# Kernel optimization log

Measured on AMD Instinct MI355X. Metric: run time of the kernel, lower is better.

## Reference

```python
import jax, jax.numpy as jnp
import numpy as np

EPSILON = 1e-6
SEARCH_RADIUS = 11 // 2  # search_window_size=11 -> 121 shifts
PATCH_RADIUS = 5 // 2    # patch_size=5 box sum


def shift_stack(t, r):
    # Matches ShiftStack: outer loop x_shift, inner loop y_shift, roll dims (H,W)=(2,3).
    # t: [B,C,H,W] -> [B,C,H,W,(2r+1)^2]
    return jnp.stack(
        [jnp.roll(t, (dy, dx), axis=(2, 3))
         for dx in range(-r, r + 1) for dy in range(-r, r + 1)],
        axis=-1,
    )


def box_sum(t, r):
    # Circular box-filter sum over a (2r+1)x(2r+1) window; separable form is
    # mathematically identical to the original 25 rolls (rolls commute/add).
    s = sum(jnp.roll(t, d, axis=2) for d in range(-r, r + 1))
    return sum(jnp.roll(s, d, axis=3) for d in range(-r, r + 1))


def setup_inputs() -> dict:
    key = jax.random.key(0)
    k1, k2 = jax.random.split(key)
    rgb = jax.random.uniform(k1, (1, 3, 512, 512), dtype=jnp.float32)
    # realistic noise std in [0.02, 0.12]
    sigma = jax.random.uniform(k2, (1, 1, 1, 1), dtype=jnp.float32) * 0.1 + 0.02
    return {"rgb": rgb, "sigma": sigma}


def reference(rgb, sigma):
    h = sigma * 2.0                                     # [B,1,1,1]
    y = 0.299 * rgb[:, :1] + 0.587 * rgb[:, 1:2] + 0.114 * rgb[:, 2:]  # [B,1,H,W]
    rgb_stack = shift_stack(rgb, SEARCH_RADIUS)         # [B,3,H,W,K]
    y_stack = shift_stack(y, SEARCH_RADIUS)             # [B,1,H,W,K]
    sq_diff = (y[..., None] - y_stack) ** 2             # [B,1,H,W,K]
    distances = jnp.sqrt(box_sum(sq_diff, PATCH_RADIUS))
    weights = jnp.exp(-distances / (jax.nn.relu(h)[..., None] + EPSILON))  # [B,1,H,W,K]
    denoised = (weights * rgb_stack).sum(axis=-1) / weights.sum(axis=-1)   # [B,3,H,W]
    return jnp.clip(denoised, 0.0, 1.0)
```

## Files before the change

### kernel.cpp

```cpp
#include <hip/hip_runtime.h>
#include <math.h>

#define IH 512
#define IW 512
#define NPX (IH*IW)
#define TS 32
#define YHALO 7
#define RHALO 5
#define YD (TS + 2*YHALO)
#define RD (TS + 2*RHALO)
#define RSZ (RD*RD)
#define NSLICE 4

#define FSQRT(x) __builtin_amdgcn_sqrtf(x)

__global__ __launch_bounds__(256)
void nlm_part(const float* __restrict__ rgb,
              const float* __restrict__ sigma,
              float4* __restrict__ ws) {
    __shared__ float Y[YD * YD];
    __shared__ float RGBL[3 * RSZ];

    const int tid = threadIdx.x;
    const int tx0 = blockIdx.x * TS;
    const int ty0 = blockIdx.y * TS;
    const int slice = blockIdx.z;

    const float* Rp = rgb;
    const float* Gp = rgb + NPX;
    const float* Bp = rgb + 2 * NPX;

    for (int idx = tid; idx < YD * YD; idx += 256) {
        int a = idx / YD, b = idx - a * YD;
        int gy = (ty0 + a - YHALO) & (IH - 1);
        int gx = (tx0 + b - YHALO) & (IW - 1);
        int g = gy * IW + gx;
        Y[idx] = 0.299f * Rp[g] + 0.587f * Gp[g] + 0.114f * Bp[g];
    }
    for (int idx = tid; idx < RSZ; idx += 256) {
        int a = idx / RD, b = idx - a * RD;
        int gy = (ty0 + a - RHALO) & (IH - 1);
        int gx = (tx0 + b - RHALO) & (IW - 1);
        int g = gy * IW + gx;
        RGBL[idx]           = Rp[g];
        RGBL[RSZ + idx]     = Gp[g];
        RGBL[2 * RSZ + idx] = Bp[g];
    }
    __syncthreads();

    const float minv_h = -1.0f / (fmaxf(sigma[0] * 2.0f, 0.0f) + 1e-6f);

    const int tx = tid & 31;
    const int tz = tid >> 5;
    const int r0 = tz * 4;

    const int ybase = (YHALO + r0 - 2) * YD + (YHALO + tx - 2);
    float yb[8][5];
    #pragma unroll
    for (int i = 0; i < 8; ++i)
        #pragma unroll
        for (int b = 0; b < 5; ++b)
            yb[i][b] = Y[ybase + i * YD + b];

    float accR[4] = {0.f, 0.f, 0.f, 0.f};
    float accG[4] = {0.f, 0.f, 0.f, 0.f};
    float accB[4] = {0.f, 0.f, 0.f, 0.f};
    float den[4]  = {0.f, 0.f, 0.f, 0.f};

    const int dxlo  = (slice < 3) ? (-5 + 3 * slice) : 4;
    const int dxcnt = (slice < 3) ? 3 : 2;

    for (int u = 0; u < dxcnt; ++u) {
        const int dx = dxlo + u;
        const int ybd = (YHALO + r0 - 7) * YD + (YHALO + tx - 2 - dx);
        const int rbd = (RHALO + r0 - 5) * RD + (RHALO + tx - dx);

        float win[8][5];
        #pragma unroll
        for (int j = 0; j < 8; ++j)
            #pragma unroll
            for (int b = 0; b < 5; ++b)
                win[j][b] = Y[ybd + j * YD + b];

        #pragma unroll
        for (int k = 0; k <= 10; ++k) {
            if (k > 0) {
                #pragma unroll
                for (int b = 0; b < 5; ++b)
                    win[(k + 7) & 7][b] = Y[ybd + (7 + k) * YD + b];
            }
            float hs[8];
            #pragma unroll
            for (int i = 0; i < 8; ++i) {
                float s = 0.f;
                #pragma unroll
                for (int b = 0; b < 5; ++b) {
                    float d = yb[i][b] - win[(i + k) & 7][b];
                    s = fmaf(d, d, s);
                }
                hs[i] = s;
            }
            float pre[9];
            pre[0] = 0.f;
            #pragma unroll
            for (int i = 0; i < 8; ++i) pre[i + 1] = pre[i] + hs[i];
            #pragma unroll
            for (int rr = 0; rr < 4; ++rr) {
                float box = pre[rr + 5] - pre[rr];
                float w = __expf(FSQRT(box) * minv_h);
                const int s2 = rbd + (rr + k) * RD;
                accR[rr] = fmaf(w, RGBL[s2], accR[rr]);
                accG[rr] = fmaf(w, RGBL[RSZ + s2], accG[rr]);
                accB[rr] = fmaf(w, RGBL[2 * RSZ + s2], accB[rr]);
                den[rr] += w;
            }
        }
    }

    #pragma unroll
    for (int rr = 0; rr < 4; ++rr) {
        int px = (ty0 + r0 + rr) * IW + tx0 + tx;
        ws[(size_t)slice * NPX + px] =
            make_float4(accR[rr], accG[rr], accB[rr], den[rr]);
    }
}

__global__ __launch_bounds__(256)
void nlm_combine(const float4* __restrict__ ws, float* __restrict__ out) {
    int px = blockIdx.x * 256 + threadIdx.x;
    float4 a = ws[px];
    float4 b = ws[NPX + px];
    float4 c = ws[2 * (size_t)NPX + px];
    float4 d = ws[3 * (size_t)NPX + px];
    float r  = a.x + b.x + c.x + d.x;
    float g  = a.y + b.y + c.y + d.y;
    float bl = a.z + b.z + c.z + d.z;
    float w  = a.w + b.w + c.w + d.w;
    float iw = 1.0f / w;
    out[px]               = fminf(fmaxf(r  * iw, 0.f), 1.f);
    out[NPX + px]         = fminf(fmaxf(g  * iw, 0.f), 1.f);
    out[2 * NPX + px]     = fminf(fmaxf(bl * iw, 0.f), 1.f);
}

__global__ __launch_bounds__(256)
void nlm_mono(const float* __restrict__ rgb,
              const float* __restrict__ sigma,
              float* __restrict__ out) {
    __shared__ float Y[YD * YD];
    __shared__ float RGBL[3 * RSZ];

    const int tid = threadIdx.x;
    const int tx0 = blockIdx.x * TS;
    const int ty0 = blockIdx.y * TS;

    const float* Rp = rgb;
    const float* Gp = rgb + NPX;
    const float* Bp = rgb + 2 * NPX;

    for (int idx = tid; idx < YD * YD; idx += 256) {
        int a = idx / YD, b = idx - a * YD;
        int gy = (ty0 + a - YHALO) & (IH - 1);
        int gx = (tx0 + b - YHALO) & (IW - 1);
        int g = gy * IW + gx;
        Y[idx] = 0.299f * Rp[g] + 0.587f * Gp[g] + 0.114f * Bp[g];
    }
    for (int idx = tid; idx < RSZ; idx += 256) {
        int a = idx / RD, b = idx - a * RD;
        int gy = (ty0 + a - RHALO) & (IH - 1);
        int gx = (tx0 + b - RHALO) & (IW - 1);
        int g = gy * IW + gx;
        RGBL[idx]           = Rp[g];
        RGBL[RSZ + idx]     = Gp[g];
        RGBL[2 * RSZ + idx] = Bp[g];
    }
    __syncthreads();

    const float minv_h = -1.0f / (fmaxf(sigma[0] * 2.0f, 0.0f) + 1e-6f);
    const int tx = tid & 31;
    const int tz = tid >> 5;
    const int r0 = tz * 4;

    const int ybase = (YHALO + r0 - 2) * YD + (YHALO + tx - 2);
    float yb[8][5];
    #pragma unroll
    for (int i = 0; i < 8; ++i)
        #pragma unroll
        for (int b = 0; b < 5; ++b)
            yb[i][b] = Y[ybase + i * YD + b];

    float accR[4] = {0.f,0.f,0.f,0.f}, accG[4] = {0.f,0.f,0.f,0.f};
    float accB[4] = {0.f,0.f,0.f,0.f}, den[4] = {0.f,0.f,0.f,0.f};

    for (int dx = -5; dx <= 5; ++dx) {
        const int ybd = (YHALO + r0 - 7) * YD + (YHALO + tx - 2 - dx);
        const int rbd = (RHALO + r0 - 5) * RD + (RHALO + tx - dx);

        float win[8][5];
        #pragma unroll
        for (int j = 0; j < 8; ++j)
            #pragma unroll
            for (int b = 0; b < 5; ++b)
                win[j][b] = Y[ybd + j * YD + b];

        #pragma unroll
        for (int k = 0; k <= 10; ++k) {
            if (k > 0) {
                #pragma unroll
                for (int b = 0; b < 5; ++b)
                    win[(k + 7) & 7][b] = Y[ybd + (7 + k) * YD + b];
            }
            float hs[8];
            #pragma unroll
            for (int i = 0; i < 8; ++i) {
                float s = 0.f;
                #pragma unroll
                for (int b = 0; b < 5; ++b) {
                    float d = yb[i][b] - win[(i + k) & 7][b];
                    s = fmaf(d, d, s);
                }
                hs[i] = s;
            }
            float pre[9];
            pre[0] = 0.f;
            #pragma unroll
            for (int i = 0; i < 8; ++i) pre[i + 1] = pre[i] + hs[i];
            #pragma unroll
            for (int rr = 0; rr < 4; ++rr) {
                float box = pre[rr + 5] - pre[rr];
                float w = __expf(FSQRT(box) * minv_h);
                const int s2 = rbd + (rr + k) * RD;
                accR[rr] = fmaf(w, RGBL[s2], accR[rr]);
                accG[rr] = fmaf(w, RGBL[RSZ + s2], accG[rr]);
                accB[rr] = fmaf(w, RGBL[2 * RSZ + s2], accB[rr]);
                den[rr] += w;
            }
        }
    }

    #pragma unroll
    for (int rr = 0; rr < 4; ++rr) {
        int px = (ty0 + r0 + rr) * IW + tx0 + tx;
        float iw = 1.0f / den[rr];
        out[px]           = fminf(fmaxf(accR[rr] * iw, 0.f), 1.f);
        out[NPX + px]     = fminf(fmaxf(accG[rr] * iw, 0.f), 1.f);
        out[2 * NPX + px] = fminf(fmaxf(accB[rr] * iw, 0.f), 1.f);
    }
}

extern "C" void kernel_launch(void* const* d_in, const int* in_sizes, int n_in,
                              void* d_out, int out_size, void* d_ws, size_t ws_size,
                              hipStream_t stream) {
    const float* rgb   = (const float*)d_in[0];
    const float* sigma = (const float*)d_in[1];
    float* out = (float*)d_out;

    const size_t need = (size_t)NSLICE * NPX * sizeof(float4);
    if (ws_size >= need) {
        float4* ws = (float4*)d_ws;
        dim3 grid(IW / TS, IH / TS, NSLICE);
        nlm_part<<<grid, dim3(256), 0, stream>>>(rgb, sigma, ws);
        nlm_combine<<<dim3(NPX / 256), dim3(256), 0, stream>>>(ws, out);
    } else {
        dim3 grid(IW / TS, IH / TS);
        nlm_mono<<<grid, dim3(256), 0, stream>>>(rgb, sigma, out);
    }
}
```

Baseline: 42.52 us.

## Expand squared difference into correlation, use float2 LDS reads and more slices

The patch SSD is rewritten as |a|^2+|b|^2-2ab, with the query norms precomputed and the window norms computed incrementally. Window values are read from shared memory as float2 using even and odd shifted copies of the luma tile. RGB values now come straight from global memory (cached) instead of an LDS tile. The dx split grows to 6 slices when workspace allows, exp is replaced by exp2 with a prescaled constant, and the combine kernel takes a variable slice count. The expansion can lose precision through cancellation, so the box sum is clamped at zero, and the extra slices add partial-sum traffic.

After: 62.08 us. +46.0%, slower.

```diff
diff --git a/kernel.cpp b/kernel.cpp
--- a/kernel.cpp
+++ b/kernel.cpp
@@ -10,27 +10,171 @@
 #define YD (TS + 2*YHALO)
 #define RD (TS + 2*RHALO)
 #define RSZ (RD*RD)
-#define NSLICE 4
+#define YSZ (YD*YD)
 
 #define FSQRT(x) __builtin_amdgcn_sqrtf(x)
+#if __has_builtin(__builtin_amdgcn_exp2f)
+#define FEXP2(x) __builtin_amdgcn_exp2f(x)
+#else
+#define FEXP2(x) exp2f(x)
+#endif
 
 __global__ __launch_bounds__(256)
 void nlm_part(const float* __restrict__ rgb,
               const float* __restrict__ sigma,
               float4* __restrict__ ws) {
-    __shared__ float Y[YD * YD];
-    __shared__ float RGBL[3 * RSZ];
+    __shared__ float Ye[YSZ];
+    __shared__ float Yo[YSZ];
 
     const int tid = threadIdx.x;
     const int tx0 = blockIdx.x * TS;
     const int ty0 = blockIdx.y * TS;
     const int slice = blockIdx.z;
+    const int nz = gridDim.z;
 
     const float* Rp = rgb;
     const float* Gp = rgb + NPX;
     const float* Bp = rgb + 2 * NPX;
 
-    for (int idx = tid; idx < YD * YD; idx += 256) {
+    for (int idx = tid; idx < YSZ; idx += 256) {
+        int a = idx / YD, b = idx - a * YD;
+        int gy = (ty0 + a - YHALO) & (IH - 1);
+        int gx = (tx0 + b - YHALO) & (IW - 1);
+        int g = gy * IW + gx;
+        float y = 0.299f * Rp[g] + 0.587f * Gp[g] + 0.114f * Bp[g];
+        Ye[idx] = y;
+        if (b > 0) Yo[idx - 1] = y;
+    }
+    __syncthreads();
+
+    const float m2 = -1.4426950408889634f /
+                     (fmaxf(sigma[0] * 2.0f, 0.0f) + 1e-6f);
+
+    const int tx = tid & 31;
+    const int tz = tid >> 5;
+    const int r0 = tz * 4;
+
+    const int ybase = (YHALO + r0 - 2) * YD + (YHALO + tx - 2);
+    float yb[8][5];
+    float ybsq[8];
+    #pragma unroll
+    for (int i = 0; i < 8; ++i) {
+        float s = 0.f;
+        #pragma unroll
+        for (int b = 0; b < 5; ++b) {
+            float v = Ye[ybase + i * YD + b];
+            yb[i][b] = v;
+            s = fmaf(v, v, s);
+        }
+        ybsq[i] = s;
+    }
+
+    int rb[14];
+    #pragma unroll
+    for (int q = 0; q < 14; ++q)
+        rb[q] = ((ty0 + r0 - 5 + q) & (IH - 1)) << 9;
+
+    float accR[4] = {0.f, 0.f, 0.f, 0.f};
+    float accG[4] = {0.f, 0.f, 0.f, 0.f};
+    float accB[4] = {0.f, 0.f, 0.f, 0.f};
+    float den[4]  = {0.f, 0.f, 0.f, 0.f};
+
+    int dxlo, dxcnt;
+    if (nz == 6) { if (slice < 5) { dxlo = -5 + 2 * slice; dxcnt = 2; }
+                   else           { dxlo = 5;              dxcnt = 1; } }
+    else         { if (slice < 3) { dxlo = -5 + 3 * slice; dxcnt = 3; }
+                   else           { dxlo = 4;              dxcnt = 2; } }
+
+    for (int u = 0; u < dxcnt; ++u) {
+        const int dx  = dxlo + u;
+        const int col = (tx0 + tx - dx) & (IW - 1);
+        const int c   = YHALO + tx - 2 - dx;
+        const float* Yb_ = (c & 1) ? Yo : Ye;
+        const int ci  = (c & 1) ? (c - 1) : c;
+        const float2* wbase =
+            reinterpret_cast<const float2*>(Yb_ + r0 * YD + ci);
+
+        float winsq[8];
+        #pragma unroll
+        for (int k = 0; k <= 10; ++k) {
+            float hs[8];
+            #pragma unroll
+            for (int i = 0; i < 8; ++i) {
+                const int j = i + k;
+                float2 w0 = wbase[j * (YD / 2) + 0];
+                float2 w1 = wbase[j * (YD / 2) + 1];
+                float2 w2 = wbase[j * (YD / 2) + 2];
+                float cr = yb[i][0] * w0.x;
+                cr = fmaf(yb[i][1], w0.y, cr);
+                cr = fmaf(yb[i][2], w1.x, cr);
+                cr = fmaf(yb[i][3], w1.y, cr);
+                cr = fmaf(yb[i][4], w2.x, cr);
+                if (k == 0 || i == 7) {
+                    float s = w0.x * w0.x;
+                    s = fmaf(w0.y, w0.y, s);
+                    s = fmaf(w1.x, w1.x, s);
+                    s = fmaf(w1.y, w1.y, s);
+                    s = fmaf(w2.x, w2.x, s);
+                    winsq[j & 7] = s;
+                }
+                hs[i] = fmaf(-2.f, cr, ybsq[i] + winsq[j & 7]);
+            }
+            float pre[9];
+            pre[0] = 0.f;
+            #pragma unroll
+            for (int i = 0; i < 8; ++i) pre[i + 1] = pre[i] + hs[i];
+            #pragma unroll
+            for (int rr = 0; rr < 4; ++rr) {
+                float box = fmaxf(pre[rr + 5] - pre[rr], 0.f);
+                float w = FEXP2(FSQRT(box) * m2);
+                const int off = rb[rr + k] + col;
+                accR[rr] = fmaf(w, Rp[off], accR[rr]);
+                accG[rr] = fmaf(w, Gp[off], accG[rr]);
+                accB[rr] = fmaf(w, Bp[off], accB[rr]);
+                den[rr] += w;
+            }
+        }
+    }
+
+    #pragma unroll
+    for (int rr = 0; rr < 4; ++rr) {
+        int px = (ty0 + r0 + rr) * IW + tx0 + tx;
+        ws[(size_t)slice * NPX + px] =
+            make_float4(accR[rr], accG[rr], accB[rr], den[rr]);
+    }
+}
+
+__global__ __launch_bounds__(256)
+void nlm_combine(const float4* __restrict__ ws, float* __restrict__ out,
+                 int nslice) {
+    int px = blockIdx.x * 256 + threadIdx.x;
+    float r = 0.f, g = 0.f, b = 0.f, w = 0.f;
+    for (int s = 0; s < nslice; ++s) {
+        float4 v = ws[(size_t)s * NPX + px];
+        r += v.x; g += v.y; b += v.z; w += v.w;
+    }
+    float iw = 1.0f / w;
+    out[px]           = fminf(fmaxf(r * iw, 0.f), 1.f);
+    out[NPX + px]     = fminf(fmaxf(g * iw, 0.f), 1.f);
+    out[2 * NPX + px] = fminf(fmaxf(b * iw, 0.f), 1.f);
+}
+
+__global__ __launch_bounds__(256)
+void nlm_mono(const float* __restrict__ rgb,
+              const float* __restrict__ sigma,
+              float* __restrict__ out) {
+    __shared__ float Y[YSZ];
+    __shared__ float RGBL[3 * RSZ];
+
+    const int tid = threadIdx.x;
+    const int tx0 = blockIdx.x * TS;
+    const int ty0 = blockIdx.y * TS;
+
+    const float* Rp = rgb;
+    const float* Gp = rgb + NPX;
+    const float* Bp = rgb + 2 * NPX;
+
+    for (int idx = tid; idx < YSZ; idx += 256) {
         int a = idx / YD, b = idx - a * YD;
         int gy = (ty0 + a - YHALO) & (IH - 1);
         int gx = (tx0 + b - YHALO) & (IW - 1);
@@ -49,7 +193,6 @@
     __syncthreads();
 
     const float minv_h = -1.0f / (fmaxf(sigma[0] * 2.0f, 0.0f) + 1e-6f);
-
     const int tx = tid & 31;
     const int tz = tid >> 5;
     const int r0 = tz * 4;
@@ -62,40 +205,22 @@
         for (int b = 0; b < 5; ++b)
             yb[i][b] = Y[ybase + i * YD + b];
 
-    float accR[4] = {0.f, 0.f, 0.f, 0.f};
-    float accG[4] = {0.f, 0.f, 0.f, 0.f};
-    float accB[4] = {0.f, 0.f, 0.f, 0.f};
-    float den[4]  = {0.f, 0.f, 0.f, 0.f};
-
-    const int dxlo  = (slice < 3) ? (-5 + 3 * slice) : 4;
-    const int dxcnt = (slice < 3) ? 3 : 2;
-
-    for (int u = 0; u < dxcnt; ++u) {
-        const int dx = dxlo + u;
+    float accR[4] = {0.f,0.f,0.f,0.f}, accG[4] = {0.f,0.f,0.f,0.f};
+    float accB[4] = {0.f,0.f,0.f,0.f}, den[4] = {0.f,0.f,0.f,0.f};
+
+    for (int dx = -5; dx <= 5; ++dx) {
         const int ybd = (YHALO + r0 - 7) * YD + (YHALO + tx - 2 - dx);
         const int rbd = (RHALO + r0 - 5) * RD + (RHALO + tx - dx);
 
-        float win[8][5];
-        #pragma unroll
-        for (int j = 0; j < 8; ++j)
-            #pragma unroll
-            for (int b = 0; b < 5; ++b)
-                win[j][b] = Y[ybd + j * YD + b];
-
         #pragma unroll
         for (int k = 0; k <= 10; ++k) {
-            if (k > 0) {
-                #pragma unroll
-                for (int b = 0; b < 5; ++b)
-                    win[(k + 7) & 7][b] = Y[ybd + (7 + k) * YD + b];
-            }
             float hs[8];
             #pragma unroll
             for (int i = 0; i < 8; ++i) {
                 float s = 0.f;
                 #pragma unroll
                 for (int b = 0; b < 5; ++b) {
-                    float d = yb[i][b] - win[(i + k) & 7][b];
+                    float d = yb[i][b] - Y[ybd + (i + k) * YD + b];
                     s = fmaf(d, d, s);
                 }
                 hs[i] = s;
@@ -120,126 +245,6 @@
     #pragma unroll
     for (int rr = 0; rr < 4; ++rr) {
         int px = (ty0 + r0 + rr) * IW + tx0 + tx;
-        ws[(size_t)slice * NPX + px] =
-            make_float4(accR[rr], accG[rr], accB[rr], den[rr]);
-    }
-}
-
-__global__ __launch_bounds__(256)
-void nlm_combine(const float4* __restrict__ ws, float* __restrict__ out) {
-    int px = blockIdx.x * 256 + threadIdx.x;
-    float4 a = ws[px];
-    float4 b = ws[NPX + px];
-    float4 c = ws[2 * (size_t)NPX + px];
-    float4 d = ws[3 * (size_t)NPX + px];
-    float r  = a.x + b.x + c.x + d.x;
-    float g  = a.y + b.y + c.y + d.y;
-    float bl = a.z + b.z + c.z + d.z;
-    float w  = a.w + b.w + c.w + d.w;
-    float iw = 1.0f / w;
-    out[px]               = fminf(fmaxf(r  * iw, 0.f), 1.f);
-    out[NPX + px]         = fminf(fmaxf(g  * iw, 0.f), 1.f);
-    out[2 * NPX + px]     = fminf(fmaxf(bl * iw, 0.f), 1.f);
-}
-
-__global__ __launch_bounds__(256)
-void nlm_mono(const float* __restrict__ rgb,
-              const float* __restrict__ sigma,
-              float* __restrict__ out) {
-    __shared__ float Y[YD * YD];
-    __shared__ float RGBL[3 * RSZ];
-
-    const int tid = threadIdx.x;
-    const int tx0 = blockIdx.x * TS;
-    const int ty0 = blockIdx.y * TS;
-
-    const float* Rp = rgb;
-    const float* Gp = rgb + NPX;
-    const float* Bp = rgb + 2 * NPX;
-
-    for (int idx = tid; idx < YD * YD; idx += 256) {
-        int a = idx / YD, b = idx - a * YD;
-        int gy = (ty0 + a - YHALO) & (IH - 1);
-        int gx = (tx0 + b - YHALO) & (IW - 1);
-        int g = gy * IW + gx;
-        Y[idx] = 0.299f * Rp[g] + 0.587f * Gp[g] + 0.114f * Bp[g];
-    }
-    for (int idx = tid; idx < RSZ; idx += 256) {
-        int a = idx / RD, b = idx - a * RD;
-        int gy = (ty0 + a - RHALO) & (IH - 1);
-        int gx = (tx0 + b - RHALO) & (IW - 1);
-        int g = gy * IW + gx;
-        RGBL[idx]           = Rp[g];
-        RGBL[RSZ + idx]     = Gp[g];
-        RGBL[2 * RSZ + idx] = Bp[g];
-    }
-    __syncthreads();
-
-    const float minv_h = -1.0f / (fmaxf(sigma[0] * 2.0f, 0.0f) + 1e-6f);
-    const int tx = tid & 31;
-    const int tz = tid >> 5;
-    const int r0 = tz * 4;
-
-    const int ybase = (YHALO + r0 - 2) * YD + (YHALO + tx - 2);
-    float yb[8][5];
-    #pragma unroll
-    for (int i = 0; i < 8; ++i)
-        #pragma unroll
-        for (int b = 0; b < 5; ++b)
-            yb[i][b] = Y[ybase + i * YD + b];
-
-    float accR[4] = {0.f,0.f,0.f,0.f}, accG[4] = {0.f,0.f,0.f,0.f};
-    float accB[4] = {0.f,0.f,0.f,0.f}, den[4] = {0.f,0.f,0.f,0.f};
-
-    for (int dx = -5; dx <= 5; ++dx) {
-        const int ybd = (YHALO + r0 - 7) * YD + (YHALO + tx - 2 - dx);
-        const int rbd = (RHALO + r0 - 5) * RD + (RHALO + tx - dx);
-
-        float win[8][5];
-        #pragma unroll
-        for (int j = 0; j < 8; ++j)
-            #pragma unroll
-            for (int b = 0; b < 5; ++b)
-                win[j][b] = Y[ybd + j * YD + b];
-
-        #pragma unroll
-        for (int k = 0; k <= 10; ++k) {
-            if (k > 0) {
-                #pragma unroll
-                for (int b = 0; b < 5; ++b)
-                    win[(k + 7) & 7][b] = Y[ybd + (7 + k) * YD + b];
-            }
-            float hs[8];
-            #pragma unroll
-            for (int i = 0; i < 8; ++i) {
-                float s = 0.f;
-                #pragma unroll
-                for (int b = 0; b < 5; ++b) {
-                    float d = yb[i][b] - win[(i + k) & 7][b];
-                    s = fmaf(d, d, s);
-                }
-                hs[i] = s;
-            }
-            float pre[9];
-            pre[0] = 0.f;
-            #pragma unroll
-            for (int i = 0; i < 8; ++i) pre[i + 1] = pre[i] + hs[i];
-            #pragma unroll
-            for (int rr = 0; rr < 4; ++rr) {
-                float box = pre[rr + 5] - pre[rr];
-                float w = __expf(FSQRT(box) * minv_h);
-                const int s2 = rbd + (rr + k) * RD;
-                accR[rr] = fmaf(w, RGBL[s2], accR[rr]);
-                accG[rr] = fmaf(w, RGBL[RSZ + s2], accG[rr]);
-                accB[rr] = fmaf(w, RGBL[2 * RSZ + s2], accB[rr]);
-                den[rr] += w;
-            }
-        }
-    }
-
-    #pragma unroll
-    for (int rr = 0; rr < 4; ++rr) {
-        int px = (ty0 + r0 + rr) * IW + tx0 + tx;
         float iw = 1.0f / den[rr];
         out[px]           = fminf(fmaxf(accR[rr] * iw, 0.f), 1.f);
         out[NPX + px]     = fminf(fmaxf(accG[rr] * iw, 0.f), 1.f);
@@ -254,12 +259,15 @@
     const float* sigma = (const float*)d_in[1];
     float* out = (float*)d_out;
 
-    const size_t need = (size_t)NSLICE * NPX * sizeof(float4);
-    if (ws_size >= need) {
+    const size_t need6 = (size_t)6 * NPX * sizeof(float4);
+    const size_t need4 = (size_t)4 * NPX * sizeof(float4);
+    int nslice = (ws_size >= need6) ? 6 : (ws_size >= need4 ? 4 : 0);
+
+    if (nslice > 0) {
         float4* ws = (float4*)d_ws;
-        dim3 grid(IW / TS, IH / TS, NSLICE);
+        dim3 grid(IW / TS, IH / TS, nslice);
         nlm_part<<<grid, dim3(256), 0, stream>>>(rgb, sigma, ws);
-        nlm_combine<<<dim3(NPX / 256), dim3(256), 0, stream>>>(ws, out);
+        nlm_combine<<<dim3(NPX / 256), dim3(256), 0, stream>>>(ws, out, nslice);
     } else {
         dim3 grid(IW / TS, IH / TS);
         nlm_mono<<<grid, dim3(256), 0, stream>>>(rgb, sigma, out);
```
